# Kernel tuning notes

Hardware: AMD Instinct MI355X
Metric: run time of the kernel (lower is better)

The kernel has to match this reference:

```python
import jax, jax.numpy as jnp
import numpy as np

PS = 8  # patch_size


def setup_inputs() -> dict:
    key = jax.random.key(0)
    k1, k2 = jax.random.split(key)
    shape = (16, 3, 512, 512)
    return {
        "input": jax.random.normal(k1, shape, dtype=jnp.float32),
        "target": jax.random.normal(k2, shape, dtype=jnp.float32),
    }


def _extract_patches(x):
    # (B,C,H,W) -> (B,C,nh,nw,ps,ps); H,W assumed divisible by PS (no pad needed)
    B, C, H, W = x.shape
    x = x.reshape(B, C, H // PS, PS, W // PS, PS)
    return jnp.transpose(x, (0, 1, 2, 4, 3, 5))


def _fft_feats(patches):
    fft = jnp.fft.fft2(patches, norm="ortho")          # over last two axes
    fft = jnp.fft.fftshift(fft, axes=(-2, -1))
    real, imag = fft.real, fft.imag
    # log1p norm: sign(x) * log1p(|x|)
    real = jnp.sign(real) * jnp.log1p(jnp.abs(real))
    imag = jnp.sign(imag) * jnp.log1p(jnp.abs(imag))
    return real, imag


def reference(input, target):
    ir, ii = _fft_feats(_extract_patches(input))
    tr, ti = _fft_feats(_extract_patches(target))
    loss = (ir - tr) ** 2 + (ii - ti) ** 2   # mse real + mse imag, unreduced
    return jnp.mean(loss)
```

## Files before the change

kernel.cpp:

```cpp
#include <hip/hip_runtime.h>

#define SQ1_2 0.70710678118654752440f

__device__ __forceinline__ float g_feat(float x) {
    return copysignf(__logf(1.0f + fabsf(x)), x);
}

__device__ __forceinline__ void rfft8(const float r[8], float o[8]) {
    float s0 = r[0] + r[4], d0 = r[0] - r[4];
    float s1 = r[1] + r[5], d1 = r[1] - r[5];
    float s2 = r[2] + r[6], d2 = r[2] - r[6];
    float s3 = r[3] + r[7], d3 = r[3] - r[7];
    float ss02 = s0 + s2, sd02 = s0 - s2;
    float ss13 = s1 + s3, sd13 = s1 - s3;
    float t1 = SQ1_2 * (d1 - d3);
    float t2 = SQ1_2 * (d1 + d3);
    o[0] = ss02 + ss13;
    o[1] = ss02 - ss13;
    o[2] = d0 + t1;
    o[3] = -(d2 + t2);
    o[4] = sd02;
    o[5] = -sd13;
    o[6] = d0 - t1;
    o[7] = d2 - t2;
}

__device__ __forceinline__ void cfft8(const float xr[8], const float xi[8],
                                      float Fr[8], float Fi[8]) {
    float s0r = xr[0] + xr[4], s0i = xi[0] + xi[4], d0r = xr[0] - xr[4], d0i = xi[0] - xi[4];
    float s1r = xr[1] + xr[5], s1i = xi[1] + xi[5], d1r = xr[1] - xr[5], d1i = xi[1] - xi[5];
    float s2r = xr[2] + xr[6], s2i = xi[2] + xi[6], d2r = xr[2] - xr[6], d2i = xi[2] - xi[6];
    float s3r = xr[3] + xr[7], s3i = xi[3] + xi[7], d3r = xr[3] - xr[7], d3i = xi[3] - xi[7];
    float ss0r = s0r + s2r, ss0i = s0i + s2i, sd0r = s0r - s2r, sd0i = s0i - s2i;
    float ss1r = s1r + s3r, ss1i = s1i + s3i, sd1r = s1r - s3r, sd1i = s1i - s3i;
    Fr[0] = ss0r + ss1r; Fi[0] = ss0i + ss1i;
    Fr[4] = ss0r - ss1r; Fi[4] = ss0i - ss1i;
    Fr[2] = sd0r + sd1i; Fi[2] = sd0i - sd1r;
    Fr[6] = sd0r - sd1i; Fi[6] = sd0i + sd1r;
    float t1r = SQ1_2 * (d1r + d1i), t1i = SQ1_2 * (d1i - d1r);
    float t2r = d2i,                 t2i = -d2r;
    float t3r = SQ1_2 * (d3i - d3r), t3i = -SQ1_2 * (d3r + d3i);
    float ts0r = d0r + t2r, ts0i = d0i + t2i, td0r = d0r - t2r, td0i = d0i - t2i;
    float ts1r = t1r + t3r, ts1i = t1i + t3i, td1r = t1r - t3r, td1i = t1i - t3i;
    Fr[1] = ts0r + ts1r; Fi[1] = ts0i + ts1i;
    Fr[5] = ts0r - ts1r; Fi[5] = ts0i - ts1i;
    Fr[3] = td0r + td1i; Fi[3] = td0i - td1r;
    Fr[7] = td0r - td1i; Fi[7] = td0i + td1r;
}

__device__ __forceinline__ void stage1(const float* __restrict__ src, long base,
                                       float v[64]) {
    #pragma unroll
    for (int m = 0; m < 8; ++m) {
        const float4* p = reinterpret_cast<const float4*>(src + base + (long)m * 512);
        float4 a = p[0];
        float4 b = p[1];
        float r[8] = {a.x * 0.125f, a.y * 0.125f, a.z * 0.125f, a.w * 0.125f,
                      b.x * 0.125f, b.y * 0.125f, b.z * 0.125f, b.w * 0.125f};
        rfft8(r, &v[m * 8]);
    }
}

__device__ __forceinline__ void stage2_feats(const float v[64], float f[64]) {
    #pragma unroll
    for (int j = 0; j < 2; ++j) {
        float c[8], o[8];
        #pragma unroll
        for (int m = 0; m < 8; ++m) c[m] = v[m * 8 + j];
        rfft8(c, o);
        #pragma unroll
        for (int k = 0; k < 8; ++k) f[j * 8 + k] = g_feat(o[k]);
    }
    #pragma unroll
    for (int l = 0; l < 3; ++l) {
        float cr[8], ci[8], Fr[8], Fi[8];
        #pragma unroll
        for (int m = 0; m < 8; ++m) {
            cr[m] = v[m * 8 + 2 + 2 * l];
            ci[m] = v[m * 8 + 3 + 2 * l];
        }
        cfft8(cr, ci, Fr, Fi);
        #pragma unroll
        for (int k = 0; k < 8; ++k) {
            f[16 + l * 16 + k]     = g_feat(Fr[k]);
            f[16 + l * 16 + 8 + k] = g_feat(Fi[k]);
        }
    }
}

__global__ __launch_bounds__(256) void patchfft_loss_kernel(
        const float* __restrict__ in, const float* __restrict__ tgt,
        float* __restrict__ out) {
    int p = blockIdx.x * 256 + threadIdx.x;
    int pw = p & 63;
    int ph = (p >> 6) & 63;
    int bc = p >> 12;
    long base = (long)bc * 262144 + ph * 4096 + pw * 8;

    float a[64];
    stage1(in, base, a);
    float f[64];
    stage2_feats(a, f);

    stage1(tgt, base, a);

    float acc1 = 0.0f, acc2 = 0.0f;
    #pragma unroll
    for (int j = 0; j < 2; ++j) {
        float c[8], o[8];
        #pragma unroll
        for (int m = 0; m < 8; ++m) c[m] = a[m * 8 + j];
        rfft8(c, o);
        {
            float d0 = f[j * 8 + 0] - g_feat(o[0]); acc1 += d0 * d0;
            float d1 = f[j * 8 + 1] - g_feat(o[1]); acc1 += d1 * d1;
        }
        #pragma unroll
        for (int k = 2; k < 8; ++k) {
            float d = f[j * 8 + k] - g_feat(o[k]); acc2 += d * d;
        }
    }
    #pragma unroll
    for (int l = 0; l < 3; ++l) {
        float cr[8], ci[8], Fr[8], Fi[8];
        #pragma unroll
        for (int m = 0; m < 8; ++m) {
            cr[m] = a[m * 8 + 2 + 2 * l];
            ci[m] = a[m * 8 + 3 + 2 * l];
        }
        cfft8(cr, ci, Fr, Fi);
        #pragma unroll
        for (int k = 0; k < 8; ++k) {
            float d = f[16 + l * 16 + k]     - g_feat(Fr[k]); acc2 += d * d;
            float e = f[16 + l * 16 + 8 + k] - g_feat(Fi[k]); acc2 += e * e;
        }
    }
    float loss = acc1 + 2.0f * acc2;

    #pragma unroll
    for (int off = 32; off > 0; off >>= 1) loss += __shfl_down(loss, off, 64);
    __shared__ float wsum[4];
    int lane = threadIdx.x & 63;
    int wid  = threadIdx.x >> 6;
    if (lane == 0) wsum[wid] = loss;
    __syncthreads();
    if (threadIdx.x == 0) {
        float s = wsum[0] + wsum[1] + wsum[2] + wsum[3];
        atomicAdd(out, s * (1.0f / 12582912.0f));
    }
}

extern "C" void kernel_launch(void* const* d_in, const int* in_sizes, int n_in,
                              void* d_out, int out_size, void* d_ws, size_t ws_size,
                              hipStream_t stream) {
    const float* in  = (const float*)d_in[0];
    const float* tgt = (const float*)d_in[1];
    float* out = (float*)d_out;
    (void)in_sizes; (void)n_in; (void)d_ws; (void)ws_size; (void)out_size;

    hipMemsetAsync(out, 0, sizeof(float), stream);
    patchfft_loss_kernel<<<768, 256, 0, stream>>>(in, tgt, out);
}
```

Measured before the change: 122.0 us.

## Split input and target patches across wave halves and pair via lane shuffles

Each wave now processes 32 patches. Lanes 0-31 transform the input patch and lanes 32-63 transform the matching target patch, and the differences are formed with a cross-half shuffle. This removes the 64-register feature buffer, which should cut register pressure and raise occupancy, and it doubles the grid. The natural log is replaced by log2, with ln2 squared folded into the final scale; the halved loss counts each difference twice, and a 0.5 factor compensates.

```diff
diff --git a/kernel.cpp b/kernel.cpp
--- a/kernel.cpp
+++ b/kernel.cpp
@@ -2,8 +2,8 @@
 
 #define SQ1_2 0.70710678118654752440f
 
-__device__ __forceinline__ float g_feat(float x) {
-    return copysignf(__logf(1.0f + fabsf(x)), x);
+__device__ __forceinline__ float g2f(float x) {
+    return copysignf(__log2f(1.0f + fabsf(x)), x);
 }
 
 __device__ __forceinline__ void rfft8(const float r[8], float o[8]) {
@@ -61,65 +61,40 @@
     }
 }
 
-__device__ __forceinline__ void stage2_feats(const float v[64], float f[64]) {
-    #pragma unroll
-    for (int j = 0; j < 2; ++j) {
-        float c[8], o[8];
-        #pragma unroll
-        for (int m = 0; m < 8; ++m) c[m] = v[m * 8 + j];
-        rfft8(c, o);
-        #pragma unroll
-        for (int k = 0; k < 8; ++k) f[j * 8 + k] = g_feat(o[k]);
-    }
-    #pragma unroll
-    for (int l = 0; l < 3; ++l) {
-        float cr[8], ci[8], Fr[8], Fi[8];
-        #pragma unroll
-        for (int m = 0; m < 8; ++m) {
-            cr[m] = v[m * 8 + 2 + 2 * l];
-            ci[m] = v[m * 8 + 3 + 2 * l];
-        }
-        cfft8(cr, ci, Fr, Fi);
-        #pragma unroll
-        for (int k = 0; k < 8; ++k) {
-            f[16 + l * 16 + k]     = g_feat(Fr[k]);
-            f[16 + l * 16 + 8 + k] = g_feat(Fi[k]);
-        }
-    }
-}
-
 __global__ __launch_bounds__(256) void patchfft_loss_kernel(
         const float* __restrict__ in, const float* __restrict__ tgt,
         float* __restrict__ out) {
-    int p = blockIdx.x * 256 + threadIdx.x;
-    int pw = p & 63;
-    int ph = (p >> 6) & 63;
-    int bc = p >> 12;
+    int tid  = blockIdx.x * 256 + threadIdx.x;
+    int lane = threadIdx.x & 63;
+    int sub  = lane & 31;
+    int half = lane >> 5;
+    int pidx = (tid >> 6) * 32 + sub;
+    int pw = pidx & 63;
+    int ph = (pidx >> 6) & 63;
+    int bc = pidx >> 12;
     long base = (long)bc * 262144 + ph * 4096 + pw * 8;
+    const float* __restrict__ src = half ? tgt : in;
 
     float a[64];
-    stage1(in, base, a);
-    float f[64];
-    stage2_feats(a, f);
-
-    stage1(tgt, base, a);
+    stage1(src, base, a);
 
     float acc1 = 0.0f, acc2 = 0.0f;
+
     #pragma unroll
     for (int j = 0; j < 2; ++j) {
         float c[8], o[8];
         #pragma unroll
         for (int m = 0; m < 8; ++m) c[m] = a[m * 8 + j];
         rfft8(c, o);
-        {
-            float d0 = f[j * 8 + 0] - g_feat(o[0]); acc1 += d0 * d0;
-            float d1 = f[j * 8 + 1] - g_feat(o[1]); acc1 += d1 * d1;
-        }
         #pragma unroll
-        for (int k = 2; k < 8; ++k) {
-            float d = f[j * 8 + k] - g_feat(o[k]); acc2 += d * d;
+        for (int k = 0; k < 8; ++k) {
+            float f = g2f(o[k]);
+            float d = f - __shfl_xor(f, 32, 64);
+            if (k < 2) acc1 += d * d;
+            else       acc2 += d * d;
         }
     }
+
     #pragma unroll
     for (int l = 0; l < 3; ++l) {
         float cr[8], ci[8], Fr[8], Fi[8];
@@ -131,22 +106,27 @@
         cfft8(cr, ci, Fr, Fi);
         #pragma unroll
         for (int k = 0; k < 8; ++k) {
-            float d = f[16 + l * 16 + k]     - g_feat(Fr[k]); acc2 += d * d;
-            float e = f[16 + l * 16 + 8 + k] - g_feat(Fi[k]); acc2 += e * e;
+            float fr = g2f(Fr[k]);
+            float fi = g2f(Fi[k]);
+            float dr = fr - __shfl_xor(fr, 32, 64);
+            float di = fi - __shfl_xor(fi, 32, 64);
+            acc2 += dr * dr + di * di;
         }
     }
+
     float loss = acc1 + 2.0f * acc2;
 
     #pragma unroll
     for (int off = 32; off > 0; off >>= 1) loss += __shfl_down(loss, off, 64);
     __shared__ float wsum[4];
-    int lane = threadIdx.x & 63;
-    int wid  = threadIdx.x >> 6;
+    int wid = threadIdx.x >> 6;
     if (lane == 0) wsum[wid] = loss;
     __syncthreads();
     if (threadIdx.x == 0) {
+        constexpr float SCALE =
+            (float)(0.5 * 0.48045301391820142467 / 12582912.0);
         float s = wsum[0] + wsum[1] + wsum[2] + wsum[3];
-        atomicAdd(out, s * (1.0f / 12582912.0f));
+        atomicAdd(out, s * SCALE);
     }
 }
 
@@ -159,5 +139,5 @@
     (void)in_sizes; (void)n_in; (void)d_ws; (void)ws_size; (void)out_size;
 
     hipMemsetAsync(out, 0, sizeof(float), stream);
-    patchfft_loss_kernel<<<768, 256, 0, stream>>>(in, tgt, out);
+    patchfft_loss_kernel<<<1536, 256, 0, stream>>>(in, tgt, out);
 }
```

Measured after the change: 123.4 us. No clear change (+1.1%).
